# Optimization experiments

Measured on AMD Instinct MI355X. Metric: run time of the kernel, lower is better.

Reference implementation:

```python
import jax, jax.numpy as jnp
import numpy as np

B, S, D, H, FF = 16, 1024, 1024, 8, 4096
DH = D // H
EPS = 1e-5

def _ln(x, g, b):
    mu = jnp.mean(x, axis=-1, keepdims=True)
    var = jnp.mean((x - mu) ** 2, axis=-1, keepdims=True)
    return (x - mu) * jax.lax.rsqrt(var + EPS) * g + b

def setup_inputs() -> dict:
    key = jax.random.key(0)
    ks = jax.random.split(key, 12)
    sd = D ** -0.5
    return {
        "x": jax.random.normal(ks[0], (B, S, D), jnp.float32),
        "bias": jax.random.normal(ks[1], (S, S), jnp.float32),
        "Wq": jax.random.normal(ks[2], (D, D), jnp.float32) * sd,
        "bq": jnp.zeros((D,), jnp.float32),
        "Wk": jax.random.normal(ks[3], (D, D), jnp.float32) * sd,
        "bk": jnp.zeros((D,), jnp.float32),
        "Wv": jax.random.normal(ks[4], (D, D), jnp.float32) * sd,
        "bv": jnp.zeros((D,), jnp.float32),
        "Wo": jax.random.normal(ks[5], (D, D), jnp.float32) * sd,
        "bo": jnp.zeros((D,), jnp.float32),
        "ln1_g": jnp.ones((D,), jnp.float32),
        "ln1_b": jnp.zeros((D,), jnp.float32),
        "W1": jax.random.normal(ks[6], (FF, D), jnp.float32) * sd,
        "b1": jnp.zeros((FF,), jnp.float32),
        "W2": jax.random.normal(ks[7], (D, FF), jnp.float32) * (FF ** -0.5),
        "b2": jnp.zeros((D,), jnp.float32),
        "ln2_g": jnp.ones((D,), jnp.float32),
        "ln2_b": jnp.zeros((D,), jnp.float32),
    }

def reference(x, bias, Wq, bq, Wk, bk, Wv, bv, Wo, bo, ln1_g, ln1_b,
              W1, b1, W2, b2, ln2_g, ln2_b):
    # torch nn.Linear: y = x @ W.T + b
    Q = x @ Wq.T + bq  # [B,S,D]
    K = x @ Wk.T + bk
    V = x @ Wv.T + bv
    # Faithful to torch: plain row-major reshape [B,S,H*dh] -> [B*H,S,dh]
    Q = Q.reshape(B * H, S, DH)
    K = K.reshape(B * H, S, DH)
    V = V.reshape(B * H, S, DH)
    scale = DH ** -0.5
    scores = jnp.einsum('bqd,bkd->bqk', Q, K)  # [B*H,S,S]
    scores = (scores + bias[None]) * scale      # bias added BEFORE scaling, as in source
    attn = jax.nn.softmax(scores, axis=-1)
    selfattention = attn[0]
    ctx = jnp.einsum('bqk,bkd->bqd', attn, V).reshape(B, S, D)
    out = ctx @ Wo.T + bo
    out = _ln(out + x, ln1_g, ln1_b)
    # FFN
    h = jax.nn.relu(out @ W1.T + b1)
    ff = h @ W2.T + b2
    out2 = _ln(ff + out, ln2_g, ln2_b)
    return out2, selfattention
```

## Files before the change

kernel.cpp:

```cpp
#include <hip/hip_runtime.h>
#include <hip/hip_bf16.h>
#include <math.h>

typedef __attribute__((ext_vector_type(4))) float f32x4;
typedef __attribute__((ext_vector_type(8))) __bf16 bf16x8;
typedef __attribute__((ext_vector_type(4))) __bf16 bf16x4;

static constexpr float SCALE = 0.08838834764831845f;
static constexpr float SCALE_LOG2E = 0.1275174482f;

__device__ __forceinline__ void load_lds16(const void* g, void* l) {
  __builtin_amdgcn_global_load_lds(
      (const __attribute__((address_space(1))) void*)g,
      (__attribute__((address_space(3))) void*)l, 16, 0, 0);
}

__global__ __launch_bounds__(256) void cast_kernel(const float* __restrict__ s,
                                                   __bf16* __restrict__ d, int n4) {
  int i = blockIdx.x * blockDim.x + threadIdx.x;
  int stride = gridDim.x * blockDim.x;
  for (; i < n4; i += stride) {
    float4 v = reinterpret_cast<const float4*>(s)[i];
    bf16x4 o;
    o[0] = (__bf16)v.x; o[1] = (__bf16)v.y; o[2] = (__bf16)v.z; o[3] = (__bf16)v.w;
    reinterpret_cast<bf16x4*>(d)[i] = o;
  }
}

__global__ __launch_bounds__(256) void cast_weights(
    const float* __restrict__ wq, const float* __restrict__ wk,
    const float* __restrict__ wv, const float* __restrict__ wo,
    const float* __restrict__ w1, const float* __restrict__ w2,
    __bf16* __restrict__ dq, __bf16* __restrict__ dk,
    __bf16* __restrict__ dv, __bf16* __restrict__ dwo,
    __bf16* __restrict__ d1, __bf16* __restrict__ d2) {
  int i = blockIdx.x * blockDim.x + threadIdx.x;
  int stride = gridDim.x * blockDim.x;
  for (; i < 3145728; i += stride) {
    const float* s; __bf16* d; int j;
    if (i < 262144)       { s = wq; d = dq;  j = i; }
    else if (i < 524288)  { s = wk; d = dk;  j = i - 262144; }
    else if (i < 786432)  { s = wv; d = dv;  j = i - 524288; }
    else if (i < 1048576) { s = wo; d = dwo; j = i - 786432; }
    else if (i < 2097152) { s = w1; d = d1;  j = i - 1048576; }
    else                  { s = w2; d = d2;  j = i - 2097152; }
    float4 v = reinterpret_cast<const float4*>(s)[j];
    bf16x4 o;
    o[0] = (__bf16)v.x; o[1] = (__bf16)v.y; o[2] = (__bf16)v.z; o[3] = (__bf16)v.w;
    reinterpret_cast<bf16x4*>(d)[j] = o;
  }
}

__global__ __launch_bounds__(256) void scale_cast_kernel(const float* __restrict__ s,
                                                         __bf16* __restrict__ d, int n4) {
  int i = blockIdx.x * blockDim.x + threadIdx.x;
  int stride = gridDim.x * blockDim.x;
  for (; i < n4; i += stride) {
    float4 v = reinterpret_cast<const float4*>(s)[i];
    bf16x4 o;
    o[0] = (__bf16)(v.x * SCALE_LOG2E); o[1] = (__bf16)(v.y * SCALE_LOG2E);
    o[2] = (__bf16)(v.z * SCALE_LOG2E); o[3] = (__bf16)(v.w * SCALE_LOG2E);
    reinterpret_cast<bf16x4*>(d)[i] = o;
  }
}

template <int EPI>
__global__ __launch_bounds__(512, 2) void gemm_bt(
    const __bf16* __restrict__ A, const __bf16* __restrict__ Bw,
    const float* __restrict__ bvec, __bf16* __restrict__ Cb,
    float* __restrict__ Cf, int M, int N, int K) {
  __shared__ __align__(16) char sm[131072];

  const int ntn = N >> 8;
  const int nwg = gridDim.x;
  const int bid = blockIdx.x;
  const int b = (bid & 7) * (nwg >> 3) + (bid >> 3);
  const int tm = b / ntn, tn = b % ntn;
  const int t = threadIdx.x, lane = t & 63;
  const int w = t >> 6;
  const int wm = w >> 2, wn = w & 3;
  const int l15 = lane & 15, lq = lane >> 4;

  f32x4 acc[8][4] = {};

  const int r0 = t >> 3;
  const int r1 = r0 + 64;
  const int kb0 = (((t & 7) << 4) ^ ((r0 & 7) << 4));
  const int wbase = w << 10;

  auto stage = [&](int kt, int p) {
    char* base = sm + (p << 16);
    const size_t kofs = (size_t)(kb0 >> 1) + ((size_t)kt << 6);
#pragma unroll
    for (int h = 0; h < 2; ++h) {
      const __bf16* gA = A + (size_t)((tm << 8) + (h << 7) + r0) * K + kofs;
      const __bf16* gA2 = A + (size_t)((tm << 8) + (h << 7) + r1) * K + kofs;
      char* lA = base + (h << 14) + wbase;
      load_lds16(gA, lA);
      load_lds16(gA2, lA + 8192);
      const __bf16* gB = Bw + (size_t)((tn << 8) + (h << 7) + r0) * K + kofs;
      const __bf16* gB2 = Bw + (size_t)((tn << 8) + (h << 7) + r1) * K + kofs;
      char* lB = base + 32768 + (h << 14) + wbase;
      load_lds16(gB, lB);
      load_lds16(gB2, lB + 8192);
    }
  };

  stage(0, 0);
  __syncthreads();

  const int NT = K >> 6;
  const int rbB = (wn & 1) << 6;
  for (int kt = 0; kt < NT; ++kt) {
    const int p = kt & 1;
    const char* Ab = sm + (p << 16) + (wm << 14);
    const char* Bb = sm + (p << 16) + 32768 + ((wn >> 1) << 14);
    if (kt + 1 < NT) stage(kt + 1, p ^ 1);

    bf16x8 bfv[4][2];
#pragma unroll
    for (int nf = 0; nf < 4; ++nf) {
      const int r = rbB + (nf << 4) + l15;
      const int sw = (r & 7) << 4;
#pragma unroll
      for (int ks = 0; ks < 2; ++ks) {
        const int lb = (ks << 6) + (lq << 4);
        bfv[nf][ks] = *(const bf16x8*)(Bb + r * 128 + (lb ^ sw));
      }
    }
#pragma unroll
    for (int q = 0; q < 4; ++q) {
      bf16x8 af[2][2];
#pragma unroll
      for (int dm = 0; dm < 2; ++dm) {
        const int r = (((q << 1) + dm) << 4) + l15;
        const int sw = (r & 7) << 4;
#pragma unroll
        for (int ks = 0; ks < 2; ++ks) {
          const int lb = (ks << 6) + (lq << 4);
          af[dm][ks] = *(const bf16x8*)(Ab + r * 128 + (lb ^ sw));
        }
      }
#pragma unroll
      for (int ks = 0; ks < 2; ++ks)
#pragma unroll
        for (int dm = 0; dm < 2; ++dm)
#pragma unroll
          for (int nf = 0; nf < 4; ++nf)
            acc[(q << 1) + dm][nf] = __builtin_amdgcn_mfma_f32_16x16x32_bf16(
                af[dm][ks], bfv[nf][ks], acc[(q << 1) + dm][nf], 0, 0, 0);
    }
    __syncthreads();
  }

  const int row0 = (tm << 8) + (wm << 7) + (lq << 2);
  const int col0 = (tn << 8) + (wn << 6) + l15;
#pragma unroll
  for (int nf = 0; nf < 4; ++nf) {
    const int col = col0 + (nf << 4);
    const float bv = bvec[col];
#pragma unroll
    for (int mf = 0; mf < 8; ++mf) {
#pragma unroll
      for (int r = 0; r < 4; ++r) {
        const int row = row0 + (mf << 4) + r;
        float v = acc[mf][nf][r] + bv;
        if (EPI == 1) v = fmaxf(v, 0.f);
        if (EPI == 2) {
          Cf[(size_t)row * N + col] = v;
        } else if (EPI == 3) {
          size_t vt = ((size_t)(row >> 7) << 17) + ((size_t)(col & 127) << 10) +
                      ((row & 127) << 3) + (col >> 7);
          Cb[vt] = (__bf16)v;
        } else {
          Cb[(size_t)row * N + col] = (__bf16)v;
        }
      }
    }
  }
}

__global__ __launch_bounds__(256) void attn_flash(
    const __bf16* __restrict__ Q, const __bf16* __restrict__ K,
    const __bf16* __restrict__ VT, const __bf16* __restrict__ biasS,
    __bf16* __restrict__ ctx) {
  __shared__ __bf16 Ks[64 * 128];
  __shared__ __bf16 VTs[128 * 64];
  __shared__ __bf16 Ps[4][16 * 64];

  const int bid = blockIdx.x;
  const int b = ((bid & 7) << 8) | (bid >> 3);
  const int g = b >> 4;
  const int q0 = (b & 15) << 6;
  const size_t goff = (size_t)g << 17;
  const __bf16* Qg = Q + goff;
  const __bf16* Kg = K + goff;
  const __bf16* VTg = VT + goff;

  const int t = threadIdx.x, w = t >> 6, lane = t & 63;
  const int l15 = lane & 15, lq = lane >> 4;
  const int qg = q0 + (w << 4) + l15;

  bf16x8 qf[4];
  {
    const __bf16* qrow = Qg + (size_t)qg * 128 + (lq << 3);
#pragma unroll
    for (int ec = 0; ec < 4; ++ec) qf[ec] = *(const bf16x8*)(qrow + (ec << 5));
  }
  const __bf16* bSr = biasS + ((size_t)qg << 10) + (lq << 2);

  float lrun = 0.f;
  f32x4 cacc[8] = {};

  for (int kb = 0; kb < 1024; kb += 64) {
    {
      int srow = lane >> 4;
      int sbo = (lane & 15) << 4;
#pragma unroll
      for (int i = 0; i < 4; ++i) {
        int c = (w << 2) + i;
        int r = (c << 2) + srow;
        int ke = (sbo ^ ((r & 7) << 4)) >> 1;
        load_lds16(Kg + (size_t)(kb + r) * 128 + ke, (char*)Ks + (c << 10));
      }
    }
    {
      int srow = lane >> 3;
      int sbo = (lane & 7) << 4;
#pragma unroll
      for (int i = 0; i < 4; ++i) {
        int c = (w << 2) + i;
        int e = (c << 3) + srow;
        int ke = kb + ((sbo ^ ((e & 7) << 4)) >> 1);
        load_lds16(VTg + (size_t)e * 1024 + ke, (char*)VTs + (c << 10));
      }
    }
    __syncthreads();

    f32x4 sacc[4] = {};
    __builtin_amdgcn_s_setprio(1);
#pragma unroll
    for (int ec = 0; ec < 4; ++ec) {
      const int lb = (ec << 6) + (lq << 4);
#pragma unroll
      for (int kn = 0; kn < 4; ++kn) {
        int rb = (kn << 4) + l15;
        bf16x8 kf = *(const bf16x8*)((const char*)Ks + rb * 256 + (lb ^ ((rb & 7) << 4)));
        sacc[kn] = __builtin_amdgcn_mfma_f32_16x16x32_bf16(kf, qf[ec], sacc[kn], 0, 0, 0);
      }
    }
    __builtin_amdgcn_s_setprio(0);

    const __bf16* bt = bSr + kb;
#pragma unroll
    for (int kn = 0; kn < 4; ++kn) {
      bf16x4 bb = *(const bf16x4*)(bt + (kn << 4));
      bf16x4 pk;
#pragma unroll
      for (int r = 0; r < 4; ++r) {
        float p = exp2f(fmaf(sacc[kn][r], SCALE_LOG2E, (float)bb[r]));
        lrun += p;
        pk[r] = (__bf16)p;
      }
      int bo = (kn << 5) + (lq << 3);
      *(bf16x4*)((char*)Ps[w] + l15 * 128 + (bo ^ ((l15 & 7) << 4))) = pk;
    }
    asm volatile("s_waitcnt lgkmcnt(0)" ::: "memory");
    __builtin_amdgcn_sched_barrier(0);

    __builtin_amdgcn_s_setprio(1);
#pragma unroll
    for (int ks = 0; ks < 2; ++ks) {
      const int lb = (ks << 6) + (lq << 4);
      bf16x8 paf = *(const bf16x8*)((const char*)Ps[w] + l15 * 128 + (lb ^ ((l15 & 7) << 4)));
#pragma unroll
      for (int et = 0; et < 8; ++et) {
        int e = (et << 4) + l15;
        bf16x8 vf = *(const bf16x8*)((const char*)VTs + e * 128 + (lb ^ ((e & 7) << 4)));
        cacc[et] = __builtin_amdgcn_mfma_f32_16x16x32_bf16(paf, vf, cacc[et], 0, 0, 0);
      }
    }
    __builtin_amdgcn_s_setprio(0);
    __syncthreads();
  }

  lrun += __shfl_xor(lrun, 16);
  lrun += __shfl_xor(lrun, 32);
  float lrunR[4];
#pragma unroll
  for (int r = 0; r < 4; ++r)
    lrunR[r] = __shfl(lrun, (lane & 48) + ((lane & 48) >> 2) + r);
  __bf16* cg = ctx + goff;
  const int qr = q0 + (w << 4) + (lq << 2);
#pragma unroll
  for (int et = 0; et < 8; ++et)
#pragma unroll
    for (int r = 0; r < 4; ++r) {
      float v = cacc[et][r] / lrunR[r];
      cg[(size_t)(qr + r) * 128 + (et << 4) + l15] = (__bf16)v;
    }
}

__global__ __launch_bounds__(256) void attn_head0(
    const __bf16* __restrict__ Q, const __bf16* __restrict__ K,
    const float* __restrict__ bias, float* __restrict__ out) {
  __shared__ float qrow[128];
  __shared__ float red[8];
  const int q = blockIdx.x, t = threadIdx.x;
  if (t < 128) qrow[t] = (float)Q[(size_t)q * 128 + t];
  __syncthreads();
  float s[4];
#pragma unroll
  for (int c = 0; c < 4; ++c) {
    int kc = (c << 8) + t;
    const __bf16* kr = K + (size_t)kc * 128;
    float dot = 0.f;
#pragma unroll
    for (int e = 0; e < 128; e += 8) {
      bf16x8 kv = *(const bf16x8*)(kr + e);
#pragma unroll
      for (int j = 0; j < 8; ++j) dot += qrow[e + j] * (float)kv[j];
    }
    s[c] = (dot + bias[(size_t)q * 1024 + kc]) * SCALE;
  }
  float mx = fmaxf(fmaxf(s[0], s[1]), fmaxf(s[2], s[3]));
#pragma unroll
  for (int d = 32; d >= 1; d >>= 1) mx = fmaxf(mx, __shfl_xor(mx, d));
  const int w = t >> 6, lane = t & 63;
  if (lane == 0) red[w] = mx;
  __syncthreads();
  mx = fmaxf(fmaxf(red[0], red[1]), fmaxf(red[2], red[3]));
  float ex[4], sum = 0.f;
#pragma unroll
  for (int c = 0; c < 4; ++c) { ex[c] = __expf(s[c] - mx); sum += ex[c]; }
#pragma unroll
  for (int d = 32; d >= 1; d >>= 1) sum += __shfl_xor(sum, d);
  __syncthreads();
  if (lane == 0) red[4 + w] = sum;
  __syncthreads();
  sum = red[4] + red[5] + red[6] + red[7];
  float inv = 1.f / sum;
#pragma unroll
  for (int c = 0; c < 4; ++c) out[(size_t)q * 1024 + (c << 8) + t] = ex[c] * inv;
}

template <int A_BF16, int B_BF16>
__global__ __launch_bounds__(256) void ln_res(
    const void* __restrict__ aptr, const void* __restrict__ bptr,
    const float* __restrict__ gam, const float* __restrict__ bet,
    float* __restrict__ outf, __bf16* __restrict__ outb) {
  __shared__ float red[8];
  const int row = blockIdx.x, t = threadIdx.x;
  const size_t base = (size_t)row << 10;
  float a0, a1, a2, a3;
  if (A_BF16) {
    bf16x4 va = reinterpret_cast<const bf16x4*>((const __bf16*)aptr + base)[t];
    a0 = (float)va[0]; a1 = (float)va[1]; a2 = (float)va[2]; a3 = (float)va[3];
  } else {
    float4 va = reinterpret_cast<const float4*>((const float*)aptr + base)[t];
    a0 = va.x; a1 = va.y; a2 = va.z; a3 = va.w;
  }
  float b0, b1, b2, b3;
  if (B_BF16) {
    bf16x4 vb = reinterpret_cast<const bf16x4*>((const __bf16*)bptr + base)[t];
    b0 = (float)vb[0]; b1 = (float)vb[1]; b2 = (float)vb[2]; b3 = (float)vb[3];
  } else {
    float4 vb = reinterpret_cast<const float4*>((const float*)bptr + base)[t];
    b0 = vb.x; b1 = vb.y; b2 = vb.z; b3 = vb.w;
  }
  float v0 = a0 + b0, v1 = a1 + b1, v2 = a2 + b2, v3 = a3 + b3;
  float s = v0 + v1 + v2 + v3;
  float qq = v0 * v0 + v1 * v1 + v2 * v2 + v3 * v3;
#pragma unroll
  for (int d = 32; d >= 1; d >>= 1) {
    s += __shfl_xor(s, d);
    qq += __shfl_xor(qq, d);
  }
  const int w = t >> 6, lane = t & 63;
  if (lane == 0) { red[w] = s; red[4 + w] = qq; }
  __syncthreads();
  s = red[0] + red[1] + red[2] + red[3];
  qq = red[4] + red[5] + red[6] + red[7];
  const float mu = s * (1.f / 1024.f);
  const float var = qq * (1.f / 1024.f) - mu * mu;
  const float rs = rsqrtf(var + 1e-5f);
  float4 g4 = reinterpret_cast<const float4*>(gam)[t];
  float4 b4 = reinterpret_cast<const float4*>(bet)[t];
  float o0 = (v0 - mu) * rs * g4.x + b4.x;
  float o1 = (v1 - mu) * rs * g4.y + b4.y;
  float o2 = (v2 - mu) * rs * g4.z + b4.z;
  float o3 = (v3 - mu) * rs * g4.w + b4.w;
  if (outf) reinterpret_cast<float4*>(outf + base)[t] = make_float4(o0, o1, o2, o3);
  if (outb) {
    bf16x4 ob;
    ob[0] = (__bf16)o0; ob[1] = (__bf16)o1; ob[2] = (__bf16)o2; ob[3] = (__bf16)o3;
    reinterpret_cast<bf16x4*>(outb + base)[t] = ob;
  }
}

extern "C" void kernel_launch(void* const* d_in, const int* in_sizes, int n_in,
                              void* d_out, int out_size, void* d_ws, size_t ws_size,
                              hipStream_t stream) {
  (void)in_sizes; (void)n_in; (void)out_size; (void)ws_size;
  const float* x    = (const float*)d_in[0];
  const float* bias = (const float*)d_in[1];
  const float* Wq   = (const float*)d_in[2];
  const float* bq   = (const float*)d_in[3];
  const float* Wk   = (const float*)d_in[4];
  const float* bk   = (const float*)d_in[5];
  const float* Wv   = (const float*)d_in[6];
  const float* bv   = (const float*)d_in[7];
  const float* Wo   = (const float*)d_in[8];
  const float* bo   = (const float*)d_in[9];
  const float* g1   = (const float*)d_in[10];
  const float* b1l  = (const float*)d_in[11];
  const float* W1   = (const float*)d_in[12];
  const float* b1f  = (const float*)d_in[13];
  const float* W2   = (const float*)d_in[14];
  const float* b2f  = (const float*)d_in[15];
  const float* g2   = (const float*)d_in[16];
  const float* b2l  = (const float*)d_in[17];

  char* ws = (char*)d_ws;
  size_t off = 0;
  auto alloc = [&](size_t bytes) {
    char* p = ws + off;
    off += (bytes + 255) & ~(size_t)255;
    return p;
  };
  __bf16* wqb  = (__bf16*)alloc(2097152);
  __bf16* wkb  = (__bf16*)alloc(2097152);
  __bf16* wvb  = (__bf16*)alloc(2097152);
  __bf16* wob  = (__bf16*)alloc(2097152);
  __bf16* w1b  = (__bf16*)alloc(8388608);
  __bf16* w2b  = (__bf16*)alloc(8388608);
  __bf16* biasS = (__bf16*)alloc(2097152);
  __bf16* xb   = (__bf16*)alloc(33554432);
  __bf16* Qb   = (__bf16*)alloc(4ull * 33554432);
  __bf16* Kb   = Qb + 16777216;
  __bf16* VTb  = Kb + 16777216;
  __bf16* ctxb = VTb + 16777216;
  __bf16* hb   = Qb;
  __bf16* res1b = xb;
  __bf16* attn_out_b = Qb;

  float* out2     = (float*)d_out;
  float* selfattn = (float*)d_out + 16777216;
  float* ff       = out2;

  cast_kernel<<<2048, 256, 0, stream>>>(x, xb, 16777216 / 4);
  cast_weights<<<2048, 256, 0, stream>>>(Wq, Wk, Wv, Wo, W1, W2,
                                         wqb, wkb, wvb, wob, w1b, w2b);
  scale_cast_kernel<<<512, 256, 0, stream>>>(bias, biasS, 1048576 / 4);

  gemm_bt<0><<<64 * 4, 512, 0, stream>>>(xb, wqb, bq, Qb, nullptr, 16384, 1024, 1024);
  gemm_bt<0><<<64 * 4, 512, 0, stream>>>(xb, wkb, bk, Kb, nullptr, 16384, 1024, 1024);
  gemm_bt<3><<<64 * 4, 512, 0, stream>>>(xb, wvb, bv, VTb, nullptr, 16384, 1024, 1024);

  attn_head0<<<1024, 256, 0, stream>>>(Qb, Kb, bias, selfattn);
  attn_flash<<<128 * 16, 256, 0, stream>>>(Qb, Kb, VTb, biasS, ctxb);

  gemm_bt<0><<<64 * 4, 512, 0, stream>>>(ctxb, wob, bo, attn_out_b, nullptr, 16384, 1024, 1024);

  ln_res<1, 1><<<16384, 256, 0, stream>>>(attn_out_b, xb, g1, b1l, nullptr, res1b);

  gemm_bt<1><<<64 * 16, 512, 0, stream>>>(res1b, w1b, b1f, hb, nullptr, 16384, 4096, 1024);
  gemm_bt<2><<<64 * 4, 512, 0, stream>>>(hb, w2b, b2f, nullptr, ff, 16384, 1024, 4096);

  ln_res<0, 1><<<16384, 256, 0, stream>>>(ff, res1b, g2, b2l, out2, nullptr);
}
```

Baseline: 755.7 us.

## Double-buffer K tiles in flash attention to overlap loads with compute

Adds a second LDS buffer for K so the next K tile is prefetched while the current tile's QK^T and softmax run. The V tile load is issued at the start of each iteration and waited on only before the PV matmul, using explicit vmcnt waits and barriers in place of __syncthreads. This is meant to hide global-to-LDS load latency behind MFMA work. The cost is extra LDS, which may lower occupancy, and hand-counted vmcnt values that must match the exact number of outstanding loads. The bias loads are also global reads, so the counts may not be exact.

```diff
diff --git a/kernel.cpp b/kernel.cpp
--- a/kernel.cpp
+++ b/kernel.cpp
@@ -184,7 +184,7 @@
     const __bf16* __restrict__ Q, const __bf16* __restrict__ K,
     const __bf16* __restrict__ VT, const __bf16* __restrict__ biasS,
     __bf16* __restrict__ ctx) {
-  __shared__ __bf16 Ks[64 * 128];
+  __shared__ __bf16 Ks[2][64 * 128];
   __shared__ __bf16 VTs[128 * 64];
   __shared__ __bf16 Ps[4][16 * 64];
 
@@ -209,34 +209,47 @@
   }
   const __bf16* bSr = biasS + ((size_t)qg << 10) + (lq << 2);
 
+  auto stageK = [&](int kb, int buf) {
+    int srow = lane >> 4;
+    int sbo = (lane & 15) << 4;
+#pragma unroll
+    for (int i = 0; i < 4; ++i) {
+      int c = (w << 2) + i;
+      int r = (c << 2) + srow;
+      int ke = (sbo ^ ((r & 7) << 4)) >> 1;
+      load_lds16(Kg + (size_t)(kb + r) * 128 + ke, (char*)Ks[buf] + (c << 10));
+    }
+  };
+  auto stageV = [&](int kb) {
+    int srow = lane >> 3;
+    int sbo = (lane & 7) << 4;
+#pragma unroll
+    for (int i = 0; i < 4; ++i) {
+      int c = (w << 2) + i;
+      int e = (c << 3) + srow;
+      int ke = kb + ((sbo ^ ((e & 7) << 4)) >> 1);
+      load_lds16(VTg + (size_t)e * 1024 + ke, (char*)VTs + (c << 10));
+    }
+  };
+
   float lrun = 0.f;
   f32x4 cacc[8] = {};
 
-  for (int kb = 0; kb < 1024; kb += 64) {
-    {
-      int srow = lane >> 4;
-      int sbo = (lane & 15) << 4;
-#pragma unroll
-      for (int i = 0; i < 4; ++i) {
-        int c = (w << 2) + i;
-        int r = (c << 2) + srow;
-        int ke = (sbo ^ ((r & 7) << 4)) >> 1;
-        load_lds16(Kg + (size_t)(kb + r) * 128 + ke, (char*)Ks + (c << 10));
-      }
-    }
-    {
-      int srow = lane >> 3;
-      int sbo = (lane & 7) << 4;
-#pragma unroll
-      for (int i = 0; i < 4; ++i) {
-        int c = (w << 2) + i;
-        int e = (c << 3) + srow;
-        int ke = kb + ((sbo ^ ((e & 7) << 4)) >> 1);
-        load_lds16(VTg + (size_t)e * 1024 + ke, (char*)VTs + (c << 10));
-      }
-    }
-    __syncthreads();
-
+  stageK(0, 0);
+
+  for (int it = 0; it < 16; ++it) {
+    const int kb = it << 6;
+    const int cur = it & 1;
+    stageV(kb);
+    if (it < 15) stageK(kb + 64, cur ^ 1);
+
+    if (it < 15)
+      asm volatile("s_waitcnt vmcnt(8)\ns_barrier" ::: "memory");
+    else
+      asm volatile("s_waitcnt vmcnt(4)\ns_barrier" ::: "memory");
+    __builtin_amdgcn_sched_barrier(0);
+
+    const char* Ksc = (const char*)Ks[cur];
     f32x4 sacc[4] = {};
     __builtin_amdgcn_s_setprio(1);
 #pragma unroll
@@ -245,7 +258,7 @@
 #pragma unroll
       for (int kn = 0; kn < 4; ++kn) {
         int rb = (kn << 4) + l15;
-        bf16x8 kf = *(const bf16x8*)((const char*)Ks + rb * 256 + (lb ^ ((rb & 7) << 4)));
+        bf16x8 kf = *(const bf16x8*)(Ksc + rb * 256 + (lb ^ ((rb & 7) << 4)));
         sacc[kn] = __builtin_amdgcn_mfma_f32_16x16x32_bf16(kf, qf[ec], sacc[kn], 0, 0, 0);
       }
     }
@@ -265,7 +278,11 @@
       int bo = (kn << 5) + (lq << 3);
       *(bf16x4*)((char*)Ps[w] + l15 * 128 + (bo ^ ((l15 & 7) << 4))) = pk;
     }
-    asm volatile("s_waitcnt lgkmcnt(0)" ::: "memory");
+
+    if (it < 15)
+      asm volatile("s_waitcnt vmcnt(4) lgkmcnt(0)\ns_barrier" ::: "memory");
+    else
+      asm volatile("s_waitcnt vmcnt(0) lgkmcnt(0)\ns_barrier" ::: "memory");
     __builtin_amdgcn_sched_barrier(0);
 
     __builtin_amdgcn_s_setprio(1);
@@ -281,7 +298,8 @@
       }
     }
     __builtin_amdgcn_s_setprio(0);
-    __syncthreads();
+
+    __builtin_amdgcn_s_barrier();
   }
 
   lrun += __shfl_xor(lrun, 16);
```

New measurement: 767.9 us. Within noise of the previous version (+1.6%).
